# Optimization experiments

Measured on AMD Instinct MI355X. Metric: run time of the kernel, lower is better.

Reference implementation:

```python
import jax, jax.numpy as jnp
import numpy as np

N = 100_000        # nodes
E = 1_600_000      # edges (avg degree 16)
D_IN = 128         # raw node feature dim
H = 64             # hidden dim
D_E = 8            # edge attr dim
C = 2              # classes for both heads (parity-game winner / strategy)


def setup_inputs() -> dict:
    key = jax.random.key(0)
    ks = jax.random.split(key, 16)
    rn = lambda k, shp, s: jax.random.normal(k, shp, jnp.float32) * s
    inv = lambda f: 1.0 / np.sqrt(f)
    return {
        "x": rn(ks[0], (N, D_IN), 1.0),
        "edge_index": jax.random.randint(ks[1], (2, E), 0, N),
        "edge_attr": rn(ks[2], (E, D_E), 1.0),
        # encode: Linear(D_IN -> H) + ReLU
        "W_enc": rn(ks[3], (D_IN, H), inv(D_IN)),
        "b_enc": jnp.zeros((H,), jnp.float32),
        # core: single-head GATConv
        "W_gat": rn(ks[4], (H, H), inv(H)),
        "a_src": rn(ks[5], (H,), inv(H)),
        "a_dst": rn(ks[6], (H,), inv(H)),
        # node_classifier: MLP H -> H -> C
        "Wn1": rn(ks[7], (H, H), inv(H)),
        "bn1": jnp.zeros((H,), jnp.float32),
        "Wn2": rn(ks[8], (H, C), inv(H)),
        "bn2": jnp.zeros((C,), jnp.float32),
        # edge_classifier: MLP (2H + D_E) -> H -> C
        "We1": rn(ks[9], (2 * H + D_E, H), inv(2 * H + D_E)),
        "be1": jnp.zeros((H,), jnp.float32),
        "We2": rn(ks[10], (H, C), inv(H)),
        "be2": jnp.zeros((C,), jnp.float32),
    }


def _gat_core(h, src, dst, W_gat, a_src, a_dst):
    # Single-head GAT layer with segment softmax over incoming edges per dst.
    hg = h @ W_gat                                    # [N, H]
    hs, hd = hg[src], hg[dst]                         # [E, H] gathers
    scores = jax.nn.leaky_relu(hs @ a_src + hd @ a_dst, 0.2)  # [E]
    m = jax.ops.segment_max(scores, dst, num_segments=N)      # [N]
    m = jnp.where(jnp.isneginf(m), 0.0, m)            # guard isolated nodes
    ex = jnp.exp(scores - m[dst])                     # [E]
    denom = jax.ops.segment_sum(ex, dst, num_segments=N)      # [N]
    alpha = ex / (denom[dst] + 1e-9)                  # [E]
    agg = jax.ops.segment_sum(alpha[:, None] * hs, dst, num_segments=N)  # [N, H]
    return jax.nn.relu(agg)


def reference(x, edge_index, edge_attr, W_enc, b_enc, W_gat, a_src, a_dst,
              Wn1, bn1, Wn2, bn2, We1, be1, We2, be2):
    src, dst = edge_index[0], edge_index[1]
    # encode
    h = jax.nn.relu(x @ W_enc + b_enc)                # [N, H]
    # core (GATConv)
    xc = _gat_core(h, src, dst, W_gat, a_src, a_dst)  # [N, H]
    # node head
    node_logits = jax.nn.relu(xc @ Wn1 + bn1) @ Wn2 + bn2        # [N, C]
    # gather src/dst + concat edge_attr, edge head
    edge_feat = jnp.concatenate([xc[src], xc[dst], edge_attr], axis=-1)  # [E, 2H+D_E]
    edge_logits = jax.nn.relu(edge_feat @ We1 + be1) @ We2 + be2  # [E, C]
    return node_logits, edge_logits
```

## Files before the change

kernel.cpp:

```cpp
#include <hip/hip_runtime.h>
#include <hip/hip_bf16.h>

#define NN   100000
#define EE   1600000
#define DIN  128
#define HH   64
#define DEA  8
#define NCLS 2
#define BSZ  128
#define NBUCK ((NN + BSZ - 1) / BSZ)
#define CAPG 2368
#define CAP  4096
#define NCHUNK 100
#define CHUNK (EE / NCHUNK)

typedef __hip_bfloat16 bf16;
typedef short  short8 __attribute__((ext_vector_type(8)));
typedef float  f32x4  __attribute__((ext_vector_type(4)));

__device__ __forceinline__ void bf2x(unsigned u, float& lo, float& hi) {
    union { unsigned i; float f; } a, b;
    a.i = u << 16; b.i = u & 0xffff0000u;
    lo = a.f; hi = b.f;
}
__device__ __forceinline__ short f2bs(float f) {
    unsigned u = __float_as_uint(f);
    return (short)((u + 0x7fffu + ((u >> 16) & 1u)) >> 16);
}
__device__ __forceinline__ short8 cvt8(float4 a, float4 b) {
    short8 r;
    r[0] = f2bs(a.x); r[1] = f2bs(a.y); r[2] = f2bs(a.z); r[3] = f2bs(a.w);
    r[4] = f2bs(b.x); r[5] = f2bs(b.y); r[6] = f2bs(b.z); r[7] = f2bs(b.w);
    return r;
}
__device__ __forceinline__ f32x4 z4() {
    f32x4 z; z[0] = 0.f; z[1] = 0.f; z[2] = 0.f; z[3] = 0.f; return z;
}

#define WE_STRIDE 136
#define WG_STRIDE 72
#define TB_STRIDE 68
__global__ __launch_bounds__(256) void k_encode(
        const float* __restrict__ x,
        const float* __restrict__ W_enc, const float* __restrict__ b_enc,
        const float* __restrict__ W_gat,
        const float* __restrict__ a_src, const float* __restrict__ a_dst,
        bf16* __restrict__ hg_, float* __restrict__ s_src, float* __restrict__ s_dst) {
    __shared__ short wencT[64 * WE_STRIDE];
    __shared__ short wgatT[64 * WG_STRIDE];
    __shared__ float tb[4][16 * TB_STRIDE];
    short* hg = (short*)hg_;
    int tid = threadIdx.x;
    for (int i = tid; i < DIN * HH; i += 256) {
        int k = i >> 6, n = i & 63;
        wencT[n * WE_STRIDE + k] = f2bs(W_enc[i]);
    }
    for (int i = tid; i < HH * HH; i += 256) {
        int k = i >> 6, n = i & 63;
        wgatT[n * WG_STRIDE + k] = f2bs(W_gat[i]);
    }
    __syncthreads();
    int w = tid >> 6, l = tid & 63, m = l & 15, h = l >> 4;
    short8 wg[2][4];
    #pragma unroll
    for (int kt = 0; kt < 2; kt++)
        #pragma unroll
        for (int nt = 0; nt < 4; nt++)
            wg[kt][nt] = *(short8*)&wgatT[(nt * 16 + m) * WG_STRIDE + kt * 32 + h * 8];
    float avs[4], avd[4], ben[4];
    #pragma unroll
    for (int nt = 0; nt < 4; nt++) {
        avs[nt] = a_src[nt * 16 + m];
        avd[nt] = a_dst[nt * 16 + m];
        ben[nt] = b_enc[nt * 16 + m];
    }
    int tp = blockIdx.x * 4 + w;
    if (tp >= NN / 32) return;
    int n0 = tp * 32;
    float* tbw = tb[w];

    f32x4 acc1[2][4];
    #pragma unroll
    for (int rt = 0; rt < 2; rt++)
        #pragma unroll
        for (int nt = 0; nt < 4; nt++) acc1[rt][nt] = z4();
    #pragma unroll
    for (int kt = 0; kt < 4; kt++) {
        short8 af[2];
        #pragma unroll
        for (int rt = 0; rt < 2; rt++) {
            const float* xp = &x[(size_t)(n0 + rt * 16 + m) * DIN + kt * 32 + h * 8];
            af[rt] = cvt8(*(const float4*)xp, *(const float4*)(xp + 4));
        }
        #pragma unroll
        for (int nt = 0; nt < 4; nt++) {
            short8 bf = *(short8*)&wencT[(nt * 16 + m) * WE_STRIDE + kt * 32 + h * 8];
            acc1[0][nt] = __builtin_amdgcn_mfma_f32_16x16x32_bf16(af[0], bf, acc1[0][nt], 0, 0, 0);
            acc1[1][nt] = __builtin_amdgcn_mfma_f32_16x16x32_bf16(af[1], bf, acc1[1][nt], 0, 0, 0);
        }
    }
    #pragma unroll
    for (int rt = 0; rt < 2; rt++) {
        #pragma unroll
        for (int nt = 0; nt < 4; nt++)
            #pragma unroll
            for (int r = 0; r < 4; r++) {
                float hv = fmaxf(acc1[rt][nt][r] + ben[nt], 0.f);
                tbw[(h * 4 + r) * TB_STRIDE + nt * 16 + m] = hv;
            }
        f32x4 acc2[4];
        #pragma unroll
        for (int nt = 0; nt < 4; nt++) acc2[nt] = z4();
        #pragma unroll
        for (int kt = 0; kt < 2; kt++) {
            const float* tp_ = &tbw[m * TB_STRIDE + kt * 32 + h * 8];
            short8 af2 = cvt8(*(const float4*)tp_, *(const float4*)(tp_ + 4));
            #pragma unroll
            for (int nt = 0; nt < 4; nt++)
                acc2[nt] = __builtin_amdgcn_mfma_f32_16x16x32_bf16(af2, wg[kt][nt], acc2[nt], 0, 0, 0);
        }
        float ps[4] = {0.f, 0.f, 0.f, 0.f}, pd[4] = {0.f, 0.f, 0.f, 0.f};
        #pragma unroll
        for (int nt = 0; nt < 4; nt++)
            #pragma unroll
            for (int r = 0; r < 4; r++) {
                float v = acc2[nt][r];
                ps[r] = fmaf(v, avs[nt], ps[r]);
                pd[r] = fmaf(v, avd[nt], pd[r]);
                hg[(size_t)(n0 + rt * 16 + h * 4 + r) * HH + nt * 16 + m] = f2bs(v);
            }
        #pragma unroll
        for (int off = 1; off < 16; off <<= 1)
            #pragma unroll
            for (int r = 0; r < 4; r++) {
                ps[r] += __shfl_xor(ps[r], off);
                pd[r] += __shfl_xor(pd[r], off);
            }
        if (m == 0) {
            *(float4*)&s_src[n0 + rt * 16 + h * 4] = make_float4(ps[0], ps[1], ps[2], ps[3]);
            *(float4*)&s_dst[n0 + rt * 16 + h * 4] = make_float4(pd[0], pd[1], pd[2], pd[3]);
        }
    }
}

__global__ __launch_bounds__(1024) void k_cscatter(
        const int* __restrict__ src, const int* __restrict__ dst,
        const float* __restrict__ edge_attr, short* __restrict__ attr16,
        int* bcur, unsigned* __restrict__ ebuf) {
    __shared__ int cnt[NBUCK];
    __shared__ int cur[NBUCK];
    int tid = threadIdx.x;
    int e0 = blockIdx.x * CHUNK;
    for (int i = tid; i < NBUCK; i += 1024) cnt[i] = 0;
    __syncthreads();
    if (attr16) {
        const float* ap = edge_attr + (size_t)e0 * DEA;
        short* op = attr16 + (size_t)e0 * DEA;
        for (int i = tid; i < CHUNK * DEA; i += 1024) op[i] = f2bs(ap[i]);
    }
    for (int i = tid; i < CHUNK; i += 1024)
        atomicAdd(&cnt[dst[e0 + i] >> 7], 1);
    __syncthreads();
    for (int i = tid; i < NBUCK; i += 1024) {
        int c = cnt[i];
        int base = c ? atomicAdd(&bcur[i], c) : 0;
        cur[i] = i * CAPG + base;
    }
    __syncthreads();
    for (int i = tid; i < CHUNK; i += 1024) {
        int dv = dst[e0 + i], sv = src[e0 + i];
        int b  = dv >> 7;
        int dl = dv & (BSZ - 1);
        int pos = atomicAdd(&cur[b], 1);
        ebuf[pos] = ((unsigned)dl << 24) | (unsigned)sv;
    }
}

__global__ __launch_bounds__(512) void k_bagg2(
        const unsigned* __restrict__ ebuf, const int* __restrict__ bcur,
        const float* __restrict__ s_src, const float* __restrict__ s_dst,
        const bf16* __restrict__ hg, bf16* __restrict__ agg_) {
    __shared__ unsigned sl[CAP];
    __shared__ int cnt[BSZ];
    __shared__ int sstart[BSZ];
    __shared__ int spos[BSZ];
    __shared__ int sscan[BSZ];
    short* agg = (short*)agg_;
    int tid = threadIdx.x;
    int b = blockIdx.x;
    int rs = b * CAPG;
    int ne = min(bcur[b], CAP);
    for (int i = tid; i < BSZ; i += 512) cnt[i] = 0;
    __syncthreads();
    for (int i = tid; i < ne; i += 512)
        atomicAdd(&cnt[ebuf[rs + i] >> 24], 1);
    __syncthreads();
    int v = (tid < BSZ) ? cnt[tid] : 0;
    if (tid < BSZ) sscan[tid] = v;
    __syncthreads();
    for (int s = 1; s < BSZ; s <<= 1) {
        int add = (tid < BSZ && tid >= s) ? sscan[tid - s] : 0;
        __syncthreads();
        if (tid < BSZ) sscan[tid] += add;
        __syncthreads();
    }
    if (tid < BSZ) { sstart[tid] = sscan[tid] - v; spos[tid] = sscan[tid] - v; }
    __syncthreads();
    for (int i = tid; i < ne; i += 512) {
        unsigned p = ebuf[rs + i];
        int dl = p >> 24;
        int q = atomicAdd(&spos[dl], 1);
        sl[q] = p & 0xFFFFFFu;
    }
    __syncthreads();
    int lane = tid & 63, wv = tid >> 6;
    int lane8 = lane & 7, grp = lane >> 3;
    for (int dl = wv; dl < BSZ; dl += 8) {
        int node = b * BSZ + dl;
        if (node >= NN) break;
        int st = sstart[dl], deg = cnt[dl];
        float sd = s_dst[node];
        float a[8] = {0.f}, denom = 0.f;
        for (int i = grp; i < deg; i += 8) {
            int sv = sl[st + i];
            float s = s_src[sv] + sd;
            s = (s >= 0.f) ? s : 0.2f * s;
            float ex = __expf(s);
            denom += ex;
            uint4 u = *(const uint4*)&hg[(size_t)sv * HH + lane8 * 8];
            float f0, f1, f2, f3, f4, f5, f6, f7;
            bf2x(u.x, f0, f1); bf2x(u.y, f2, f3);
            bf2x(u.z, f4, f5); bf2x(u.w, f6, f7);
            a[0] = fmaf(ex, f0, a[0]); a[1] = fmaf(ex, f1, a[1]);
            a[2] = fmaf(ex, f2, a[2]); a[3] = fmaf(ex, f3, a[3]);
            a[4] = fmaf(ex, f4, a[4]); a[5] = fmaf(ex, f5, a[5]);
            a[6] = fmaf(ex, f6, a[6]); a[7] = fmaf(ex, f7, a[7]);
        }
        #pragma unroll
        for (int off = 8; off < 64; off <<= 1) {
            #pragma unroll
            for (int j = 0; j < 8; j++) a[j] += __shfl_xor(a[j], off);
            denom += __shfl_xor(denom, off);
        }
        if (lane < 8) {
            float inv = 1.f / (denom + 1e-9f);
            short8 r;
            #pragma unroll
            for (int j = 0; j < 8; j++) r[j] = f2bs(a[j] * inv);
            *(short8*)&agg[(size_t)node * HH + lane8 * 8] = r;
        }
    }
}

#define WC_STRIDE 72
__global__ __launch_bounds__(256) void k_nodehead(
        const bf16* __restrict__ agg_,
        const float* __restrict__ Wn1, const float* __restrict__ bn1,
        const float* __restrict__ Wn2, const float* __restrict__ bn2,
        const float* __restrict__ We1,
        bf16* __restrict__ p_src_, bf16* __restrict__ p_dst_, float* __restrict__ out_node) {
    __shared__ short wcatT[192 * WC_STRIDE];
    const short* agg = (const short*)agg_;
    short* p_src = (short*)p_src_;
    short* p_dst = (short*)p_dst_;
    int tid = threadIdx.x;
    for (int i = tid; i < 3 * HH * HH; i += 256) {
        int mat = i >> 12, j = i & 4095;
        int k = j >> 6, l2 = j & 63;
        float v = (mat == 0) ? Wn1[j] : (mat == 1 ? We1[j] : We1[HH * HH + j]);
        wcatT[(mat * 64 + l2) * WC_STRIDE + k] = f2bs(v);
    }
    __syncthreads();
    int w = tid >> 6, l = tid & 63, m = l & 15, h = l >> 4;
    int tp = blockIdx.x * 4 + w;
    if (tp >= NN / 32) return;
    int n0 = tp * 32;
    float ben[4], wn2a[4], wn2b[4];
    #pragma unroll
    for (int nt = 0; nt < 4; nt++) {
        ben[nt]  = bn1[nt * 16 + m];
        wn2a[nt] = Wn2[(nt * 16 + m) * NCLS + 0];
        wn2b[nt] = Wn2[(nt * 16 + m) * NCLS + 1];
    }
    float bn20 = bn2[0], bn21 = bn2[1];
    #pragma unroll
    for (int rt = 0; rt < 2; rt++) {
        f32x4 acc[12];
        #pragma unroll
        for (int nt = 0; nt < 12; nt++) acc[nt] = z4();
        #pragma unroll
        for (int kt = 0; kt < 2; kt++) {
            short8 v = *(const short8*)&agg[(size_t)(n0 + rt * 16 + m) * HH + kt * 32 + h * 8];
            short8 af;
            #pragma unroll
            for (int j = 0; j < 8; j++) af[j] = (v[j] < 0) ? (short)0 : v[j];
            #pragma unroll
            for (int nt = 0; nt < 12; nt++) {
                short8 bf = *(short8*)&wcatT[(nt * 16 + m) * WC_STRIDE + kt * 32 + h * 8];
                acc[nt] = __builtin_amdgcn_mfma_f32_16x16x32_bf16(af, bf, acc[nt], 0, 0, 0);
            }
        }
        float l0[4] = {0.f, 0.f, 0.f, 0.f}, l1[4] = {0.f, 0.f, 0.f, 0.f};
        #pragma unroll
        for (int nt = 0; nt < 4; nt++)
            #pragma unroll
            for (int r = 0; r < 4; r++) {
                float t = fmaxf(acc[nt][r] + ben[nt], 0.f);
                l0[r] = fmaf(t, wn2a[nt], l0[r]);
                l1[r] = fmaf(t, wn2b[nt], l1[r]);
            }
        #pragma unroll
        for (int nt = 0; nt < 4; nt++)
            #pragma unroll
            for (int r = 0; r < 4; r++) {
                size_t row = (size_t)(n0 + rt * 16 + h * 4 + r) * HH + nt * 16 + m;
                p_src[row] = f2bs(acc[nt + 4][r]);
                p_dst[row] = f2bs(acc[nt + 8][r]);
            }
        #pragma unroll
        for (int off = 1; off < 16; off <<= 1)
            #pragma unroll
            for (int r = 0; r < 4; r++) {
                l0[r] += __shfl_xor(l0[r], off);
                l1[r] += __shfl_xor(l1[r], off);
            }
        if (m == 0) {
            #pragma unroll
            for (int r = 0; r < 4; r++)
                *(float2*)&out_node[(size_t)(n0 + rt * 16 + h * 4 + r) * NCLS] =
                    make_float2(l0[r] + bn20, l1[r] + bn21);
        }
    }
}

template<bool A16>
__global__ __launch_bounds__(256) void k_edgehead(
        const int* __restrict__ src, const int* __restrict__ dst,
        const float* __restrict__ edge_attr, const short* __restrict__ attr16,
        const bf16* __restrict__ p_src, const bf16* __restrict__ p_dst,
        const float* __restrict__ We1, const float* __restrict__ be1,
        const float* __restrict__ We2, const float* __restrict__ be2,
        float* __restrict__ out_edge) {
    int tid = threadIdx.x;
    int lane16 = tid & 15;
    int grp    = (tid & 63) >> 4;
    int wave   = tid >> 6;
    float w1a[DEA][4], w2c0[4], w2c1[4], b1v[4];
    #pragma unroll
    for (int d = 0; d < DEA; d++) {
        float4 v = *(const float4*)&We1[(2 * HH + d) * HH + lane16 * 4];
        w1a[d][0] = v.x; w1a[d][1] = v.y; w1a[d][2] = v.z; w1a[d][3] = v.w;
    }
    float4 bv = *(const float4*)&be1[lane16 * 4];
    b1v[0] = bv.x; b1v[1] = bv.y; b1v[2] = bv.z; b1v[3] = bv.w;
    #pragma unroll
    for (int j = 0; j < 4; j++) {
        w2c0[j] = We2[(lane16 * 4 + j) * NCLS + 0];
        w2c1[j] = We2[(lane16 * 4 + j) * NCLS + 1];
    }
    float be20 = be2[0], be21 = be2[1];

    int stride = gridDim.x * 64;
    for (int e = blockIdx.x * 64 + wave * 16 + grp * 4; e < EE; e += stride) {
        int sv[4], dv[4];
        #pragma unroll
        for (int q = 0; q < 4; q++) { sv[q] = src[e + q]; dv[q] = dst[e + q]; }
        uint2 us[4], ud[4];
        uint4 ua[4];
        float4 at0[4], at1[4];
        #pragma unroll
        for (int q = 0; q < 4; q++) {
            us[q] = *(const uint2*)&p_src[(size_t)sv[q] * HH + lane16 * 4];
            ud[q] = *(const uint2*)&p_dst[(size_t)dv[q] * HH + lane16 * 4];
            if constexpr (A16) {
                ua[q] = *(const uint4*)&attr16[(size_t)(e + q) * DEA];
            } else {
                at0[q] = *(const float4*)&edge_attr[(size_t)(e + q) * DEA];
                at1[q] = *(const float4*)&edge_attr[(size_t)(e + q) * DEA + 4];
            }
        }
        float l0[4], l1[4];
        #pragma unroll
        for (int q = 0; q < 4; q++) {
            float s0, s1, s2, s3, d0, d1, d2, d3;
            bf2x(us[q].x, s0, s1); bf2x(us[q].y, s2, s3);
            bf2x(ud[q].x, d0, d1); bf2x(ud[q].y, d2, d3);
            float t[4] = {s0 + d0 + b1v[0], s1 + d1 + b1v[1],
                          s2 + d2 + b1v[2], s3 + d3 + b1v[3]};
            float av[DEA];
            if constexpr (A16) {
                bf2x(ua[q].x, av[0], av[1]); bf2x(ua[q].y, av[2], av[3]);
                bf2x(ua[q].z, av[4], av[5]); bf2x(ua[q].w, av[6], av[7]);
            } else {
                av[0] = at0[q].x; av[1] = at0[q].y; av[2] = at0[q].z; av[3] = at0[q].w;
                av[4] = at1[q].x; av[5] = at1[q].y; av[6] = at1[q].z; av[7] = at1[q].w;
            }
            l0[q] = 0.f; l1[q] = 0.f;
            #pragma unroll
            for (int j = 0; j < 4; j++) {
                #pragma unroll
                for (int d = 0; d < DEA; d++) t[j] = fmaf(av[d], w1a[d][j], t[j]);
                float r = fmaxf(t[j], 0.f);
                l0[q] = fmaf(r, w2c0[j], l0[q]);
                l1[q] = fmaf(r, w2c1[j], l1[q]);
            }
        }
        #pragma unroll
        for (int off = 8; off; off >>= 1)
            #pragma unroll
            for (int q = 0; q < 4; q++) {
                l0[q] += __shfl_xor(l0[q], off);
                l1[q] += __shfl_xor(l1[q], off);
            }
        if (lane16 == 0) {
            #pragma unroll
            for (int q = 0; q < 4; q++)
                *(float2*)&out_edge[(size_t)(e + q) * NCLS] =
                    make_float2(l0[q] + be20, l1[q] + be21);
        }
    }
}

extern "C" void kernel_launch(void* const* d_in, const int* in_sizes, int n_in,
                              void* d_out, int out_size, void* d_ws, size_t ws_size,
                              hipStream_t stream) {
    const float* x      = (const float*)d_in[0];
    const int*   ei     = (const int*)  d_in[1];
    const float* attr   = (const float*)d_in[2];
    const float* W_enc  = (const float*)d_in[3];
    const float* b_enc  = (const float*)d_in[4];
    const float* W_gat  = (const float*)d_in[5];
    const float* a_src  = (const float*)d_in[6];
    const float* a_dst  = (const float*)d_in[7];
    const float* Wn1    = (const float*)d_in[8];
    const float* bn1    = (const float*)d_in[9];
    const float* Wn2    = (const float*)d_in[10];
    const float* bn2    = (const float*)d_in[11];
    const float* We1    = (const float*)d_in[12];
    const float* be1    = (const float*)d_in[13];
    const float* We2    = (const float*)d_in[14];
    const float* be2    = (const float*)d_in[15];
    float* out = (float*)d_out;
    float* ws  = (float*)d_ws;

    bf16*     hg_psrc = (bf16*)ws;
    bf16*     agg     = (bf16*)(ws + (size_t)NN * 32);
    bf16*     p_dst   = (bf16*)(ws + (size_t)NN * 64);
    float*    ssrc    = ws + (size_t)NN * 96;
    float*    sdst    = ssrc + NN;
    int*      bcur    = (int*)(sdst + NN);
    unsigned* ebuf    = (unsigned*)(bcur + 1024);
    short*    attr16  = (short*)(ebuf + (size_t)NBUCK * CAPG);
    size_t    need    = (size_t)((char*)(attr16 + (size_t)EE * DEA) - (char*)ws);
    bool      a16     = ws_size >= need;

    const int* srcp = ei;
    const int* dstp = ei + EE;

    hipMemsetAsync(bcur, 0, NBUCK * sizeof(int), stream);
    k_encode  <<<782, 256, 0, stream>>>(x, W_enc, b_enc, W_gat, a_src, a_dst,
                                        hg_psrc, ssrc, sdst);
    k_cscatter<<<NCHUNK, 1024, 0, stream>>>(srcp, dstp, attr, a16 ? attr16 : nullptr,
                                            bcur, ebuf);
    k_bagg2   <<<NBUCK, 512, 0, stream>>>(ebuf, bcur, ssrc, sdst, hg_psrc, agg);
    k_nodehead<<<782, 256, 0, stream>>>(agg, Wn1, bn1, Wn2, bn2, We1,
                                        hg_psrc , p_dst, out);
    if (a16)
        k_edgehead<true><<<8192, 256, 0, stream>>>(srcp, dstp, attr, attr16,
                                                   hg_psrc, p_dst, We1, be1, We2, be2,
                                                   out + (size_t)NN * NCLS);
    else
        k_edgehead<false><<<8192, 256, 0, stream>>>(srcp, dstp, attr, nullptr,
                                                    hg_psrc, p_dst, We1, be1, We2, be2,
                                                    out + (size_t)NN * NCLS);
}
```

Before: 212.8 us.

## Fuse node head into bucket aggregation kernel and split attr conversion

Merges the node-classifier/edge-projection MFMA stage into the per-bucket aggregation kernel, so aggregated features stay in LDS instead of going to global memory and being read back. The attr-to-bf16 conversion moves out of the scatter kernel into its own vectorized kernel, which slims the serial 100-block scatter. In exchange the aggregation kernel uses much more LDS (weights plus aggregate tile), which may lower occupancy, and every bucket block reloads and transposes the weights. One extra kernel launch is added.

Result: slower. 218.2 us (+2.5%).

```diff
diff --git a/kernel.cpp b/kernel.cpp
--- a/kernel.cpp
+++ b/kernel.cpp
@@ -143,9 +143,18 @@
     }
 }
 
+__global__ __launch_bounds__(256) void k_cvt(const float* __restrict__ attr,
+                                             short* __restrict__ attr16) {
+    int i = blockIdx.x * blockDim.x + threadIdx.x;
+    int stride = gridDim.x * blockDim.x;
+    for (int j = i; j < EE * DEA / 8; j += stride) {
+        const float4* p = (const float4*)(attr + (size_t)j * 8);
+        *(short8*)(attr16 + (size_t)j * 8) = cvt8(p[0], p[1]);
+    }
+}
+
 __global__ __launch_bounds__(1024) void k_cscatter(
         const int* __restrict__ src, const int* __restrict__ dst,
-        const float* __restrict__ edge_attr, short* __restrict__ attr16,
         int* bcur, unsigned* __restrict__ ebuf) {
     __shared__ int cnt[NBUCK];
     __shared__ int cur[NBUCK];
@@ -153,11 +162,6 @@
     int e0 = blockIdx.x * CHUNK;
     for (int i = tid; i < NBUCK; i += 1024) cnt[i] = 0;
     __syncthreads();
-    if (attr16) {
-        const float* ap = edge_attr + (size_t)e0 * DEA;
-        short* op = attr16 + (size_t)e0 * DEA;
-        for (int i = tid; i < CHUNK * DEA; i += 1024) op[i] = f2bs(ap[i]);
-    }
     for (int i = tid; i < CHUNK; i += 1024)
         atomicAdd(&cnt[dst[e0 + i] >> 7], 1);
     __syncthreads();
@@ -176,18 +180,31 @@
     }
 }
 
-__global__ __launch_bounds__(512) void k_bagg2(
+#define WC_STRIDE 72
+#define AGG_STRIDE 72
+__global__ __launch_bounds__(512) void k_baggnode(
         const unsigned* __restrict__ ebuf, const int* __restrict__ bcur,
         const float* __restrict__ s_src, const float* __restrict__ s_dst,
-        const bf16* __restrict__ hg, bf16* __restrict__ agg_) {
+        const bf16* __restrict__ hg,
+        const float* __restrict__ Wn1, const float* __restrict__ bn1,
+        const float* __restrict__ Wn2, const float* __restrict__ bn2,
+        const float* __restrict__ We1,
+        bf16* __restrict__ p_src_, bf16* __restrict__ p_dst_,
+        float* __restrict__ out_node) {
+    __shared__ short wcatT[192 * WC_STRIDE];
+    __shared__ short aggL[BSZ * AGG_STRIDE];
     __shared__ unsigned sl[CAP];
-    __shared__ int cnt[BSZ];
-    __shared__ int sstart[BSZ];
-    __shared__ int spos[BSZ];
-    __shared__ int sscan[BSZ];
-    short* agg = (short*)agg_;
+    __shared__ int cnt[BSZ], sstart[BSZ], spos[BSZ], sscan[BSZ];
+    short* p_src = (short*)p_src_;
+    short* p_dst = (short*)p_dst_;
     int tid = threadIdx.x;
     int b = blockIdx.x;
+    for (int i = tid; i < 3 * HH * HH; i += 512) {
+        int mat = i >> 12, j = i & 4095;
+        int k = j >> 6, l2 = j & 63;
+        float v = (mat == 0) ? Wn1[j] : (mat == 1 ? We1[j] : We1[HH * HH + j]);
+        wcatT[(mat * 64 + l2) * WC_STRIDE + k] = f2bs(v);
+    }
     int rs = b * CAPG;
     int ne = min(bcur[b], CAP);
     for (int i = tid; i < BSZ; i += 512) cnt[i] = 0;
@@ -247,34 +264,13 @@
             short8 r;
             #pragma unroll
             for (int j = 0; j < 8; j++) r[j] = f2bs(a[j] * inv);
-            *(short8*)&agg[(size_t)node * HH + lane8 * 8] = r;
-        }
-    }
-}
-
-#define WC_STRIDE 72
-__global__ __launch_bounds__(256) void k_nodehead(
-        const bf16* __restrict__ agg_,
-        const float* __restrict__ Wn1, const float* __restrict__ bn1,
-        const float* __restrict__ Wn2, const float* __restrict__ bn2,
-        const float* __restrict__ We1,
-        bf16* __restrict__ p_src_, bf16* __restrict__ p_dst_, float* __restrict__ out_node) {
-    __shared__ short wcatT[192 * WC_STRIDE];
-    const short* agg = (const short*)agg_;
-    short* p_src = (short*)p_src_;
-    short* p_dst = (short*)p_dst_;
-    int tid = threadIdx.x;
-    for (int i = tid; i < 3 * HH * HH; i += 256) {
-        int mat = i >> 12, j = i & 4095;
-        int k = j >> 6, l2 = j & 63;
-        float v = (mat == 0) ? Wn1[j] : (mat == 1 ? We1[j] : We1[HH * HH + j]);
-        wcatT[(mat * 64 + l2) * WC_STRIDE + k] = f2bs(v);
-    }
-    __syncthreads();
-    int w = tid >> 6, l = tid & 63, m = l & 15, h = l >> 4;
-    int tp = blockIdx.x * 4 + w;
-    if (tp >= NN / 32) return;
-    int n0 = tp * 32;
+            *(short8*)&aggL[dl * AGG_STRIDE + lane8 * 8] = r;
+        }
+    }
+    __syncthreads();
+    int m = lane & 15, h = lane >> 4;
+    int node16 = b * BSZ + wv * 16;
+    if (node16 >= NN) return;
     float ben[4], wn2a[4], wn2b[4];
     #pragma unroll
     for (int nt = 0; nt < 4; nt++) {
@@ -283,53 +279,50 @@
         wn2b[nt] = Wn2[(nt * 16 + m) * NCLS + 1];
     }
     float bn20 = bn2[0], bn21 = bn2[1];
-    #pragma unroll
-    for (int rt = 0; rt < 2; rt++) {
-        f32x4 acc[12];
-        #pragma unroll
-        for (int nt = 0; nt < 12; nt++) acc[nt] = z4();
-        #pragma unroll
-        for (int kt = 0; kt < 2; kt++) {
-            short8 v = *(const short8*)&agg[(size_t)(n0 + rt * 16 + m) * HH + kt * 32 + h * 8];
-            short8 af;
-            #pragma unroll
-            for (int j = 0; j < 8; j++) af[j] = (v[j] < 0) ? (short)0 : v[j];
-            #pragma unroll
-            for (int nt = 0; nt < 12; nt++) {
-                short8 bf = *(short8*)&wcatT[(nt * 16 + m) * WC_STRIDE + kt * 32 + h * 8];
-                acc[nt] = __builtin_amdgcn_mfma_f32_16x16x32_bf16(af, bf, acc[nt], 0, 0, 0);
-            }
-        }
-        float l0[4] = {0.f, 0.f, 0.f, 0.f}, l1[4] = {0.f, 0.f, 0.f, 0.f};
-        #pragma unroll
-        for (int nt = 0; nt < 4; nt++)
-            #pragma unroll
-            for (int r = 0; r < 4; r++) {
-                float t = fmaxf(acc[nt][r] + ben[nt], 0.f);
-                l0[r] = fmaf(t, wn2a[nt], l0[r]);
-                l1[r] = fmaf(t, wn2b[nt], l1[r]);
-            }
-        #pragma unroll
-        for (int nt = 0; nt < 4; nt++)
-            #pragma unroll
-            for (int r = 0; r < 4; r++) {
-                size_t row = (size_t)(n0 + rt * 16 + h * 4 + r) * HH + nt * 16 + m;
-                p_src[row] = f2bs(acc[nt + 4][r]);
-                p_dst[row] = f2bs(acc[nt + 8][r]);
-            }
-        #pragma unroll
-        for (int off = 1; off < 16; off <<= 1)
-            #pragma unroll
-            for (int r = 0; r < 4; r++) {
-                l0[r] += __shfl_xor(l0[r], off);
-                l1[r] += __shfl_xor(l1[r], off);
-            }
-        if (m == 0) {
-            #pragma unroll
-            for (int r = 0; r < 4; r++)
-                *(float2*)&out_node[(size_t)(n0 + rt * 16 + h * 4 + r) * NCLS] =
-                    make_float2(l0[r] + bn20, l1[r] + bn21);
-        }
+    f32x4 acc[12];
+    #pragma unroll
+    for (int nt = 0; nt < 12; nt++) acc[nt] = z4();
+    #pragma unroll
+    for (int kt = 0; kt < 2; kt++) {
+        short8 av = *(const short8*)&aggL[(wv * 16 + m) * AGG_STRIDE + kt * 32 + h * 8];
+        short8 af;
+        #pragma unroll
+        for (int j = 0; j < 8; j++) af[j] = (av[j] < 0) ? (short)0 : av[j];
+        #pragma unroll
+        for (int nt = 0; nt < 12; nt++) {
+            short8 bf = *(short8*)&wcatT[(nt * 16 + m) * WC_STRIDE + kt * 32 + h * 8];
+            acc[nt] = __builtin_amdgcn_mfma_f32_16x16x32_bf16(af, bf, acc[nt], 0, 0, 0);
+        }
+    }
+    float l0[4] = {0.f, 0.f, 0.f, 0.f}, l1[4] = {0.f, 0.f, 0.f, 0.f};
+    #pragma unroll
+    for (int nt = 0; nt < 4; nt++)
+        #pragma unroll
+        for (int r = 0; r < 4; r++) {
+            float t = fmaxf(acc[nt][r] + ben[nt], 0.f);
+            l0[r] = fmaf(t, wn2a[nt], l0[r]);
+            l1[r] = fmaf(t, wn2b[nt], l1[r]);
+        }
+    #pragma unroll
+    for (int nt = 0; nt < 4; nt++)
+        #pragma unroll
+        for (int r = 0; r < 4; r++) {
+            size_t row = (size_t)(node16 + h * 4 + r) * HH + nt * 16 + m;
+            p_src[row] = f2bs(acc[nt + 4][r]);
+            p_dst[row] = f2bs(acc[nt + 8][r]);
+        }
+    #pragma unroll
+    for (int off = 1; off < 16; off <<= 1)
+        #pragma unroll
+        for (int r = 0; r < 4; r++) {
+            l0[r] += __shfl_xor(l0[r], off);
+            l1[r] += __shfl_xor(l1[r], off);
+        }
+    if (m == 0) {
+        #pragma unroll
+        for (int r = 0; r < 4; r++)
+            *(float2*)&out_node[(size_t)(node16 + h * 4 + r) * NCLS] =
+                make_float2(l0[r] + bn20, l1[r] + bn21);
     }
 }
 
@@ -443,8 +436,8 @@
     float* out = (float*)d_out;
     float* ws  = (float*)d_ws;
 
-    bf16*     hg_psrc = (bf16*)ws;
-    bf16*     agg     = (bf16*)(ws + (size_t)NN * 32);
+    bf16*     hg      = (bf16*)ws;
+    bf16*     p_src   = (bf16*)(ws + (size_t)NN * 32);
     bf16*     p_dst   = (bf16*)(ws + (size_t)NN * 64);
     float*    ssrc    = ws + (size_t)NN * 96;
     float*    sdst    = ssrc + NN;
@@ -459,18 +452,19 @@
 
     hipMemsetAsync(bcur, 0, NBUCK * sizeof(int), stream);
     k_encode  <<<782, 256, 0, stream>>>(x, W_enc, b_enc, W_gat, a_src, a_dst,
-                                        hg_psrc, ssrc, sdst);
-    k_cscatter<<<NCHUNK, 1024, 0, stream>>>(srcp, dstp, attr, a16 ? attr16 : nullptr,
-                                            bcur, ebuf);
-    k_bagg2   <<<NBUCK, 512, 0, stream>>>(ebuf, bcur, ssrc, sdst, hg_psrc, agg);
-    k_nodehead<<<782, 256, 0, stream>>>(agg, Wn1, bn1, Wn2, bn2, We1,
-                                        hg_psrc , p_dst, out);
+                                        hg, ssrc, sdst);
+    if (a16)
+        k_cvt <<<2048, 256, 0, stream>>>(attr, attr16);
+    k_cscatter<<<NCHUNK, 1024, 0, stream>>>(srcp, dstp, bcur, ebuf);
+    k_baggnode<<<NBUCK, 512, 0, stream>>>(ebuf, bcur, ssrc, sdst, hg,
+                                          Wn1, bn1, Wn2, bn2, We1,
+                                          p_src, p_dst, out);
     if (a16)
         k_edgehead<true><<<8192, 256, 0, stream>>>(srcp, dstp, attr, attr16,
-                                                   hg_psrc, p_dst, We1, be1, We2, be2,
+                                                   p_src, p_dst, We1, be1, We2, be2,
                                                    out + (size_t)NN * NCLS);
     else
         k_edgehead<false><<<8192, 256, 0, stream>>>(srcp, dstp, attr, nullptr,
-                                                    hg_psrc, p_dst, We1, be1, We2, be2,
+                                                    p_src, p_dst, We1, be1, We2, be2,
                                                     out + (size_t)NN * NCLS);
 }
```
